# Kernel optimization log

Hardware: AMD Instinct MI355X
Metric: run time of the kernel (lower is better)

## Reference

```python
import jax, jax.numpy as jnp
import numpy as np

EMB = 256
HEADS = 2
IMG = 224
P1, P2 = 16, 8
LN_EPS = 1e-5


def _layer_norm(t, g, b):
    m = jnp.mean(t, axis=-1, keepdims=True)
    v = jnp.mean((t - m) ** 2, axis=-1, keepdims=True)
    return (t - m) * jax.lax.rsqrt(v + LN_EPS) * g + b


def _patch_embed(x, W, b, cls_tok, p):
    B, C, H, Wd = x.shape
    h, w = H // p, Wd // p
    # b c (h p1)(w p2) -> b (h w) (p1 p2 c)
    t = x.reshape(B, C, h, p, w, p).transpose(0, 2, 4, 3, 5, 1).reshape(B, h * w, p * p * C)
    t = t @ W + b
    cls = jnp.broadcast_to(cls_tok, (B, 1, cls_tok.shape[-1]))
    return jnp.concatenate([cls, t], axis=1)


def setup_inputs() -> dict:
    key = jax.random.key(0)
    ks = jax.random.split(key, 16)
    s = 0.02
    d = {
        "x": jax.random.normal(ks[0], (128, 3, IMG, IMG), dtype=jnp.float32),
        "W1": jax.random.normal(ks[1], (P1 * P1 * 3, EMB), dtype=jnp.float32) * s,
        "b1": jnp.zeros((EMB,), jnp.float32),
        "cls1": jax.random.normal(ks[2], (1, 1, EMB), dtype=jnp.float32),
        "W2": jax.random.normal(ks[3], (P2 * P2 * 3, EMB), dtype=jnp.float32) * s,
        "b2": jnp.zeros((EMB,), jnp.float32),
        "cls2": jax.random.normal(ks[4], (1, 1, EMB), dtype=jnp.float32),
        "ln1_g": jnp.ones((EMB,), jnp.float32),
        "ln1_b": jnp.zeros((EMB,), jnp.float32),
        "Wq": jax.random.normal(ks[5], (EMB, EMB), dtype=jnp.float32) * s,
        "bq": jnp.zeros((EMB,), jnp.float32),
        "Wk": jax.random.normal(ks[6], (EMB, EMB), dtype=jnp.float32) * s,
        "bk": jnp.zeros((EMB,), jnp.float32),
        "Wv": jax.random.normal(ks[7], (EMB, EMB), dtype=jnp.float32) * s,
        "bv": jnp.zeros((EMB,), jnp.float32),
        "Wp": jax.random.normal(ks[8], (EMB, EMB), dtype=jnp.float32) * s,
        "bp": jnp.zeros((EMB,), jnp.float32),
        "ln2_g": jnp.ones((EMB,), jnp.float32),
        "ln2_b": jnp.zeros((EMB,), jnp.float32),
        "lnc_g": jnp.ones((EMB,), jnp.float32),
        "lnc_b": jnp.zeros((EMB,), jnp.float32),
        "Wc": jax.random.normal(ks[9], (EMB, 2), dtype=jnp.float32) * s,
        "bc": jnp.zeros((2,), jnp.float32),
    }
    return d


def reference(x, W1, b1, cls1, W2, b2, cls2, ln1_g, ln1_b, Wq, bq, Wk, bk, Wv, bv,
              Wp, bp, ln2_g, ln2_b, lnc_g, lnc_b, Wc, bc):
    B = x.shape[0]
    p1 = _patch_embed(x, W1, b1, cls1, P1)   # [B, 197, 256]
    p2 = _patch_embed(x, W2, b2, cls2, P2)   # [B, 785, 256]
    n = p1.shape[1]
    idx = jnp.linspace(0.0, p2.shape[1] - 1, n).astype(jnp.int32)  # truncation like .long()
    p2r = p2[:, idx, :]
    z = jnp.concatenate([p2r, p1], axis=1)   # [B, 394, 256]
    N = z.shape[1]

    h = _layer_norm(z, ln1_g, ln1_b)
    dh = EMB // HEADS
    q = (h @ Wq + bq).reshape(B, N, HEADS, dh).transpose(0, 2, 1, 3)
    k = (h @ Wk + bk).reshape(B, N, HEADS, dh).transpose(0, 2, 1, 3)
    v = (h @ Wv + bv).reshape(B, N, HEADS, dh).transpose(0, 2, 1, 3)
    attn = jnp.einsum('bhqd,bhkd->bhqk', q, k)
    # NOTE: faithful to source — softmax of UNscaled logits, then divide by sqrt(emb)
    attn = jax.nn.softmax(attn, axis=-1) / (EMB ** 0.5)
    o = jnp.einsum('bhqk,bhkd->bhqd', attn, v).transpose(0, 2, 1, 3).reshape(B, N, EMB)
    o = o @ Wp + bp
    o = _layer_norm(o, ln2_g, ln2_b)
    z = z + o

    pooled = jnp.mean(z, axis=1)
    logits = _layer_norm(pooled, lnc_g, lnc_b) @ Wc + bc
    return jax.nn.log_softmax(logits, axis=1)
```

## Files before the change

### kernel.cpp

```cpp
#include <hip/hip_runtime.h>

typedef short short8 __attribute__((ext_vector_type(8)));
typedef float f32x4 __attribute__((ext_vector_type(4)));
typedef unsigned short us4 __attribute__((ext_vector_type(4)));
typedef unsigned short u16;

#define MFMA(a,b,c) __builtin_amdgcn_mfma_f32_16x16x32_bf16((a),(b),(c),0,0,0)

__device__ __forceinline__ u16 f2b(float f) {
    union { float f; unsigned int i; } v; v.f = f;
    unsigned int x = v.i;
    return (u16)((x + 0x7fffu + ((x >> 16) & 1u)) >> 16);
}

__device__ __forceinline__ unsigned int pk2(float lo, float hi) {
    return (unsigned int)f2b(lo) | ((unsigned int)f2b(hi) << 16);
}

__global__ __launch_bounds__(256) void k_wtrans(const float* __restrict__ W1,
        const float* __restrict__ W2, const float* __restrict__ Wq, const float* __restrict__ Wk,
        const float* __restrict__ Wv, const float* __restrict__ Wp,
        u16* __restrict__ w1t, u16* __restrict__ w2t, u16* __restrict__ wqt,
        u16* __restrict__ wkt, u16* __restrict__ wvt, u16* __restrict__ wpt) {
    int bx = blockIdx.x, n = threadIdx.x;
    if (bx < 768) {
        int k = bx, c = k % 3, t = k / 3, pj = t & 15, pi = t >> 4;
        int kp2 = c*256 + pi*16 + pj;
        w1t[(size_t)(kp2 >> 5)*8192 + n*32 + (kp2 & 31)] = f2b(W1[(size_t)k*256 + n]);
    } else if (bx < 960) {
        int k = bx - 768, c = k % 3, t = k / 3, pj = t & 7, pi = t >> 3;
        int kp2 = c*64 + pi*8 + pj;
        w2t[(size_t)(kp2 >> 5)*8192 + n*32 + (kp2 & 31)] = f2b(W2[(size_t)k*256 + n]);
    } else if (bx < 1216) { int k = bx - 960;  wqt[(size_t)(k>>5)*8192 + n*32 + (k&31)] = f2b(Wq[(size_t)k*256 + n]); }
    else if (bx < 1472)   { int k = bx - 1216; wkt[(size_t)(k>>5)*8192 + n*32 + (k&31)] = f2b(Wk[(size_t)k*256 + n]); }
    else if (bx < 1728)   { int k = bx - 1472; wvt[(size_t)(k>>5)*8192 + n*32 + (k&31)] = f2b(Wv[(size_t)k*256 + n]); }
    else                  { int k = bx - 1728; wpt[(size_t)(k>>5)*8192 + n*32 + (k&31)] = f2b(Wp[(size_t)k*256 + n]); }
}

__global__ __launch_bounds__(256) void k_cls(const float* __restrict__ cls1,
        const float* __restrict__ cls2, const float* __restrict__ g1, const float* __restrict__ be1,
        float* __restrict__ z, u16* __restrict__ h) {
    __shared__ float red[16];
    int b = blockIdx.x, e = threadIdx.x, lane = e & 63, w = e >> 6;
    float v0 = cls2[e], v1 = cls1[e];
    z[((size_t)b*394 + 0)*256 + e]   = v0;
    z[((size_t)b*394 + 197)*256 + e] = v1;
    float s0 = v0, q0 = v0*v0, s1 = v1, q1 = v1*v1;
    #pragma unroll
    for (int m = 1; m < 64; m <<= 1) {
        s0 += __shfl_xor(s0, m); q0 += __shfl_xor(q0, m);
        s1 += __shfl_xor(s1, m); q1 += __shfl_xor(q1, m);
    }
    if (lane == 0) { red[w] = s0; red[4+w] = q0; red[8+w] = s1; red[12+w] = q1; }
    __syncthreads();
    float S0 = red[0]+red[1]+red[2]+red[3],   Q0 = red[4]+red[5]+red[6]+red[7];
    float S1 = red[8]+red[9]+red[10]+red[11], Q1 = red[12]+red[13]+red[14]+red[15];
    float m0 = S0*(1.f/256.f), r0 = rsqrtf(Q0*(1.f/256.f) - m0*m0 + 1e-5f);
    float m1 = S1*(1.f/256.f), r1 = rsqrtf(Q1*(1.f/256.f) - m1*m1 + 1e-5f);
    h[((size_t)b*394 + 0)*256 + e]   = f2b((v0-m0)*r0*g1[e] + be1[e]);
    h[((size_t)b*394 + 197)*256 + e] = f2b((v1-m1)*r1*g1[e] + be1[e]);
}

__global__ __launch_bounds__(256) void k_im2col1(const float* __restrict__ x,
        u16* __restrict__ A1) {
    int b = blockIdx.y, g = blockIdx.x, tid = threadIdx.x;
    int p = tid >> 4, pi = tid & 15;
    int j = g*16 + p;
    u16* dst = A1 + ((size_t)b*208 + j)*768;
    if (j < 196) {
        int hi = j / 14, wi = j - hi*14;
        #pragma unroll
        for (int c = 0; c < 3; ++c) {
            const float* src = x + (((size_t)b*3 + c)*224 + hi*16 + pi)*224 + wi*16;
            f32x4 r0 = *(const f32x4*)(src);
            f32x4 r1 = *(const f32x4*)(src + 4);
            f32x4 r2 = *(const f32x4*)(src + 8);
            f32x4 r3 = *(const f32x4*)(src + 12);
            union { u16 u[16]; uint4 q[2]; } t;
            #pragma unroll
            for (int s = 0; s < 4; ++s) {
                t.u[s] = f2b(r0[s]); t.u[4+s] = f2b(r1[s]);
                t.u[8+s] = f2b(r2[s]); t.u[12+s] = f2b(r3[s]);
            }
            *(uint4*)&dst[c*256 + pi*16] = t.q[0];
            *(uint4*)&dst[c*256 + pi*16 + 8] = t.q[1];
        }
    } else {
        uint4 zer = {0,0,0,0};
        #pragma unroll
        for (int c = 0; c < 3; ++c) {
            *(uint4*)&dst[c*256 + pi*16] = zer;
            *(uint4*)&dst[c*256 + pi*16 + 8] = zer;
        }
    }
}

__global__ __launch_bounds__(256) void k_embed1(const u16* __restrict__ A1,
        const u16* __restrict__ w1t, const float* __restrict__ b1,
        const float* __restrict__ g1, const float* __restrict__ be1,
        float* __restrict__ z, u16* __restrict__ h, int nrows) {
    __shared__ __align__(16) u16 Ab[2][64*40];
    __shared__ __align__(16) u16 Bb[2][256*40];
    __shared__ float red[64][8];
    int tid = threadIdx.x;
    int r0 = blockIdx.x * 64;
    int w = tid >> 6, lane = tid & 63, quad = lane >> 4, tf = lane & 15;
    int arow = tid >> 2, aoff = (tid & 3) * 8;
    const u16* ap = A1 + (size_t)(r0 + arow)*768 + aoff;
    uint4 ra  = *(const uint4*)(ap);
    uint4 rb0 = *(const uint4*)&w1t[tid*8];
    uint4 rb1 = *(const uint4*)&w1t[2048 + tid*8];
    uint4 rb2 = *(const uint4*)&w1t[4096 + tid*8];
    uint4 rb3 = *(const uint4*)&w1t[6144 + tid*8];
    f32x4 zero = {0.f,0.f,0.f,0.f};
    f32x4 acc[4][4];
    #pragma unroll
    for (int m = 0; m < 4; ++m)
        #pragma unroll
        for (int nf = 0; nf < 4; ++nf) acc[m][nf] = zero;
    #pragma unroll
    for (int kc = 0; kc < 24; ++kc) {
        int buf = kc & 1;
        *(uint4*)&Ab[buf][arow*40 + aoff] = ra;
        *(uint4*)&Bb[buf][(arow      )*40 + aoff] = rb0;
        *(uint4*)&Bb[buf][(arow +  64)*40 + aoff] = rb1;
        *(uint4*)&Bb[buf][(arow + 128)*40 + aoff] = rb2;
        *(uint4*)&Bb[buf][(arow + 192)*40 + aoff] = rb3;
        int nc = kc < 23 ? kc + 1 : 23;
        ra = *(const uint4*)(ap + nc*32);
        const u16* src = w1t + (size_t)nc*8192;
        rb0 = *(const uint4*)&src[tid*8];
        rb1 = *(const uint4*)&src[2048 + tid*8];
        rb2 = *(const uint4*)&src[4096 + tid*8];
        rb3 = *(const uint4*)&src[6144 + tid*8];
        __syncthreads();
        short8 a0 = *(const short8*)&Ab[buf][(     tf)*40 + quad*8];
        short8 a1 = *(const short8*)&Ab[buf][(16 + tf)*40 + quad*8];
        short8 a2 = *(const short8*)&Ab[buf][(32 + tf)*40 + quad*8];
        short8 a3 = *(const short8*)&Ab[buf][(48 + tf)*40 + quad*8];
        #pragma unroll
        for (int nf = 0; nf < 4; ++nf) {
            short8 bb = *(const short8*)&Bb[buf][(w*64 + nf*16 + tf)*40 + quad*8];
            acc[0][nf] = MFMA(a0, bb, acc[0][nf]);
            acc[1][nf] = MFMA(a1, bb, acc[1][nf]);
            acc[2][nf] = MFMA(a2, bb, acc[2][nf]);
            acc[3][nf] = MFMA(a3, bb, acc[3][nf]);
        }
    }
    float bias[4], gv[4], bev[4];
    #pragma unroll
    for (int nf = 0; nf < 4; ++nf) {
        int n = w*64 + nf*16 + tf;
        bias[nf] = b1[n]; gv[nf] = g1[n]; bev[nf] = be1[n];
    }
    #pragma unroll
    for (int m = 0; m < 4; ++m)
        #pragma unroll
        for (int nf = 0; nf < 4; ++nf)
            #pragma unroll
            for (int i = 0; i < 4; ++i) acc[m][nf][i] += bias[nf];
    #pragma unroll
    for (int m = 0; m < 4; ++m)
        #pragma unroll
        for (int i = 0; i < 4; ++i) {
            float s = acc[m][0][i] + acc[m][1][i] + acc[m][2][i] + acc[m][3][i];
            float qv = acc[m][0][i]*acc[m][0][i] + acc[m][1][i]*acc[m][1][i]
                     + acc[m][2][i]*acc[m][2][i] + acc[m][3][i]*acc[m][3][i];
            #pragma unroll
            for (int d = 1; d < 16; d <<= 1) { s += __shfl_xor(s, d); qv += __shfl_xor(qv, d); }
            if (tf == 0) {
                red[m*16 + quad*4 + i][w] = s;
                red[m*16 + quad*4 + i][4 + w] = qv;
            }
        }
    __syncthreads();
    #pragma unroll
    for (int m = 0; m < 4; ++m)
        #pragma unroll
        for (int i = 0; i < 4; ++i) {
            int rl = m*16 + quad*4 + i;
            float S = red[rl][0]+red[rl][1]+red[rl][2]+red[rl][3];
            float Q = red[rl][4]+red[rl][5]+red[rl][6]+red[rl][7];
            float mean = S*(1.f/256.f);
            float rs = rsqrtf(Q*(1.f/256.f) - mean*mean + 1e-5f);
            int row = r0 + rl;
            if (row < nrows) {
                int img = row / 208;
                int j = row - img*208;
                if (j < 196) {
                    size_t base = ((size_t)img*394 + 198 + j)*256;
                    #pragma unroll
                    for (int nf = 0; nf < 4; ++nf) {
                        int n = w*64 + nf*16 + tf;
                        float v = acc[m][nf][i];
                        z[base + n] = v;
                        h[base + n] = f2b((v - mean)*rs*gv[nf] + bev[nf]);
                    }
                }
            }
        }
}

__global__ __launch_bounds__(256) void k_embed2(const float* __restrict__ x,
        const u16* __restrict__ w2t, const float* __restrict__ b2,
        const float* __restrict__ g1, const float* __restrict__ be1,
        float* __restrict__ z, u16* __restrict__ h) {
    __shared__ __align__(16) u16 A[16*200];
    __shared__ __align__(16) u16 Wst[8192];
    __shared__ __align__(16) float S[16*260];
    int b = blockIdx.y, g = blockIdx.x, tid = threadIdx.x;
    int p = tid >> 4, s16 = tid & 15;
    int pi = s16 >> 1, ph = s16 & 1;
    int it = g*16 + p + 1;
    uint4 wr0 = *(const uint4*)&w2t[tid*8];
    uint4 wr1 = *(const uint4*)&w2t[2048 + tid*8];
    uint4 wr2 = *(const uint4*)&w2t[4096 + tid*8];
    uint4 wr3 = *(const uint4*)&w2t[6144 + tid*8];
    auto stage = [&](const u16* base, int chunk) {
        __syncthreads();
        *(uint4*)&Wst[tid*8] = wr0;
        *(uint4*)&Wst[2048 + tid*8] = wr1;
        *(uint4*)&Wst[4096 + tid*8] = wr2;
        *(uint4*)&Wst[6144 + tid*8] = wr3;
        __syncthreads();
        if (base) {
            const u16* src = base + (size_t)chunk*8192;
            wr0 = *(const uint4*)&src[tid*8];
            wr1 = *(const uint4*)&src[2048 + tid*8];
            wr2 = *(const uint4*)&src[4096 + tid*8];
            wr3 = *(const uint4*)&src[6144 + tid*8];
        }
    };
    if (it <= 196) {
        int patch = 4*it - 1;
        int hi = patch / 28, wi = patch - hi*28;
        #pragma unroll
        for (int c = 0; c < 3; ++c) {
            const float* src = x + (((size_t)b*3 + c)*224 + hi*8 + pi)*224 + wi*8 + ph*4;
            f32x4 r = *(const f32x4*)src;
            us4 o; o[0] = f2b(r[0]); o[1] = f2b(r[1]); o[2] = f2b(r[2]); o[3] = f2b(r[3]);
            *(us4*)&A[p*200 + c*64 + pi*8 + ph*4] = o;
        }
    } else {
        us4 zer = {0,0,0,0};
        #pragma unroll
        for (int c = 0; c < 3; ++c)
            *(us4*)&A[p*200 + c*64 + pi*8 + ph*4] = zer;
    }
    int w = tid >> 6, lane = tid & 63, quad = lane >> 4, tf = lane & 15;
    f32x4 zero = {0.f,0.f,0.f,0.f};
    f32x4 acc[4] = {zero,zero,zero,zero};
    #pragma unroll
    for (int ks = 0; ks < 6; ++ks) {
        stage(ks < 5 ? w2t : nullptr, ks + 1);
        short8 a = *(const short8*)&A[tf*200 + ks*32 + quad*8];
        #pragma unroll
        for (int nf = 0; nf < 4; ++nf) {
            short8 bb = *(const short8*)&Wst[(w*64 + nf*16 + tf)*32 + quad*8];
            acc[nf] = MFMA(a, bb, acc[nf]);
        }
    }
    #pragma unroll
    for (int nf = 0; nf < 4; ++nf) {
        int n = w*64 + nf*16 + tf;
        float bias = b2[n];
        #pragma unroll
        for (int i = 0; i < 4; ++i)
            S[(quad*4 + i)*260 + n] = acc[nf][i] + bias;
    }
    __syncthreads();
    #pragma unroll
    for (int rr = 0; rr < 4; ++rr) {
        int row = w*4 + rr;
        int it2 = g*16 + row + 1;
        f32x4 v = *(const f32x4*)&S[row*260 + lane*4];
        float s = v[0]+v[1]+v[2]+v[3];
        float sq = v[0]*v[0]+v[1]*v[1]+v[2]*v[2]+v[3]*v[3];
        #pragma unroll
        for (int m = 1; m < 64; m <<= 1) { s += __shfl_xor(s, m); sq += __shfl_xor(sq, m); }
        float mean = s*(1.f/256.f);
        float rs = rsqrtf(sq*(1.f/256.f) - mean*mean + 1e-5f);
        if (it2 <= 196) {
            size_t base = ((size_t)b*394 + it2)*256 + lane*4;
            *(f32x4*)&z[base] = v;
            us4 ho;
            #pragma unroll
            for (int c = 0; c < 4; ++c) {
                int e = lane*4 + c;
                ho[c] = f2b((v[c]-mean)*rs*g1[e] + be1[e]);
            }
            *(us4*)&h[base] = ho;
        }
    }
}

__device__ __forceinline__ void store_qk(f32x4 acc[4][4], const float* __restrict__ bs,
        u16* __restrict__ dst, u16* Sst, int b, int mt, int w, int quad, int tf, int tid) {
    #pragma unroll
    for (int m = 0; m < 4; ++m) {
        __syncthreads();
        #pragma unroll
        for (int nf = 0; nf < 4; ++nf) {
            int e = w*64 + nf*16 + tf;
            float bias = bs[e];
            #pragma unroll
            for (int i = 0; i < 4; ++i) {
                int n = mt*64 + m*16 + quad*4 + i;
                Sst[(quad*4 + i)*264 + e] = (n < 394) ? f2b(acc[m][nf][i] + bias) : (u16)0;
            }
        }
        __syncthreads();
        int row = tid >> 4, c16 = tid & 15;
        int n = mt*64 + m*16 + row;
        if (n < 416) {
            int e0 = c16*16, hh = e0 >> 7, d0 = e0 & 127;
            uint4 v0 = *(const uint4*)&Sst[row*264 + e0];
            uint4 v1 = *(const uint4*)&Sst[row*264 + e0 + 8];
            u16* p = dst + ((size_t)(b*2 + hh)*416 + n)*128 + d0;
            *(uint4*)p = v0;
            *(uint4*)(p + 8) = v1;
        }
    }
}

__device__ __forceinline__ void store_v(f32x4 acc[4][4], const float* __restrict__ bs,
        u16* __restrict__ vt, u16* Sst, int b, int mt, int w, int quad, int tf, int tid) {
    #pragma unroll
    for (int nf = 0; nf < 4; ++nf) {
        __syncthreads();
        #pragma unroll
        for (int i = 0; i < 4; ++i) {
            int e = w*64 + nf*16 + quad*4 + i;
            float bias = bs[e];
            #pragma unroll
            for (int m = 0; m < 4; ++m) {
                int n = mt*64 + m*16 + tf;
                Sst[(w*16 + quad*4 + i)*72 + m*16 + tf] = (n < 394) ? f2b(acc[m][nf][i] + bias) : (u16)0;
            }
        }
        __syncthreads();
        #pragma unroll
        for (int k = 0; k < 2; ++k) {
            int ch = tid + k*256;
            int row = ch >> 3, c8 = ch & 7;
            int n0 = mt*64 + c8*8;
            if (n0 < 416) {
                int e = (row >> 4)*64 + nf*16 + (row & 15);
                int d = e & 127, hh = e >> 7;
                uint4 v = *(const uint4*)&Sst[row*72 + c8*8];
                *(uint4*)&vt[((size_t)(b*2 + hh)*128 + d)*416 + n0] = v;
            }
        }
    }
}

__global__ __launch_bounds__(256) void k_qkv(const u16* __restrict__ h,
        const u16* __restrict__ wqt, const u16* __restrict__ wkt, const u16* __restrict__ wvt,
        const float* __restrict__ bq, const float* __restrict__ bk, const float* __restrict__ bv,
        u16* __restrict__ q, u16* __restrict__ kb, u16* __restrict__ vt) {
    __shared__ __align__(16) u16 A[64*264];
    __shared__ __align__(16) u16 Wst[2][8192];
    __shared__ __align__(16) u16 Sst[4608];
    int mt = blockIdx.x, b = blockIdx.y, tid = threadIdx.x;
    uint4 wr0 = *(const uint4*)&wqt[tid*8];
    uint4 wr1 = *(const uint4*)&wqt[2048 + tid*8];
    uint4 wr2 = *(const uint4*)&wqt[4096 + tid*8];
    uint4 wr3 = *(const uint4*)&wqt[6144 + tid*8];
    auto wwrite = [&](int buf) {
        *(uint4*)&Wst[buf][tid*8] = wr0;
        *(uint4*)&Wst[buf][2048 + tid*8] = wr1;
        *(uint4*)&Wst[buf][4096 + tid*8] = wr2;
        *(uint4*)&Wst[buf][6144 + tid*8] = wr3;
    };
    auto wload = [&](const u16* src) {
        wr0 = *(const uint4*)&src[tid*8];
        wr1 = *(const uint4*)&src[2048 + tid*8];
        wr2 = *(const uint4*)&src[4096 + tid*8];
        wr3 = *(const uint4*)&src[6144 + tid*8];
    };
    #pragma unroll
    for (int it = 0; it < 8; ++it) {
        int idx = tid + it*256;
        int row = idx >> 5, seg = idx & 31;
        int n = mt*64 + row;
        uint4 val = {0,0,0,0};
        if (n < 394) val = *(const uint4*)&h[((size_t)b*394 + n)*256 + seg*8];
        *(uint4*)&A[row*264 + seg*8] = val;
    }
    int w = tid >> 6, lane = tid & 63, quad = lane >> 4, tf = lane & 15;
    f32x4 zero = {0.f,0.f,0.f,0.f};

    {
        f32x4 acc[4][4];
        #pragma unroll
        for (int m = 0; m < 4; ++m)
            #pragma unroll
            for (int nf = 0; nf < 4; ++nf) acc[m][nf] = zero;
        #pragma unroll
        for (int ks = 0; ks < 8; ++ks) {
            int buf = ks & 1;
            wwrite(buf);
            wload(ks < 7 ? wqt + (size_t)(ks+1)*8192 : wkt);
            __syncthreads();
            short8 a0 = *(const short8*)&A[tf*264 + ks*32 + quad*8];
            short8 a1 = *(const short8*)&A[(16+tf)*264 + ks*32 + quad*8];
            short8 a2 = *(const short8*)&A[(32+tf)*264 + ks*32 + quad*8];
            short8 a3 = *(const short8*)&A[(48+tf)*264 + ks*32 + quad*8];
            #pragma unroll
            for (int nf = 0; nf < 4; ++nf) {
                short8 bb = *(const short8*)&Wst[buf][(w*64 + nf*16 + tf)*32 + quad*8];
                acc[0][nf] = MFMA(a0, bb, acc[0][nf]);
                acc[1][nf] = MFMA(a1, bb, acc[1][nf]);
                acc[2][nf] = MFMA(a2, bb, acc[2][nf]);
                acc[3][nf] = MFMA(a3, bb, acc[3][nf]);
            }
        }
        store_qk(acc, bq, q, Sst, b, mt, w, quad, tf, tid);
    }
    {
        f32x4 acc[4][4];
        #pragma unroll
        for (int m = 0; m < 4; ++m)
            #pragma unroll
            for (int nf = 0; nf < 4; ++nf) acc[m][nf] = zero;
        #pragma unroll
        for (int ks = 0; ks < 8; ++ks) {
            int buf = ks & 1;
            wwrite(buf);
            wload(ks < 7 ? wkt + (size_t)(ks+1)*8192 : wvt);
            __syncthreads();
            short8 a0 = *(const short8*)&A[tf*264 + ks*32 + quad*8];
            short8 a1 = *(const short8*)&A[(16+tf)*264 + ks*32 + quad*8];
            short8 a2 = *(const short8*)&A[(32+tf)*264 + ks*32 + quad*8];
            short8 a3 = *(const short8*)&A[(48+tf)*264 + ks*32 + quad*8];
            #pragma unroll
            for (int nf = 0; nf < 4; ++nf) {
                short8 bb = *(const short8*)&Wst[buf][(w*64 + nf*16 + tf)*32 + quad*8];
                acc[0][nf] = MFMA(a0, bb, acc[0][nf]);
                acc[1][nf] = MFMA(a1, bb, acc[1][nf]);
                acc[2][nf] = MFMA(a2, bb, acc[2][nf]);
                acc[3][nf] = MFMA(a3, bb, acc[3][nf]);
            }
        }
        store_qk(acc, bk, kb, Sst, b, mt, w, quad, tf, tid);
    }
    {
        f32x4 acc[4][4];
        #pragma unroll
        for (int m = 0; m < 4; ++m)
            #pragma unroll
            for (int nf = 0; nf < 4; ++nf) acc[m][nf] = zero;
        #pragma unroll
        for (int ks = 0; ks < 8; ++ks) {
            int buf = ks & 1;
            wwrite(buf);
            if (ks < 7) wload(wvt + (size_t)(ks+1)*8192);
            __syncthreads();
            short8 a0 = *(const short8*)&A[tf*264 + ks*32 + quad*8];
            short8 a1 = *(const short8*)&A[(16+tf)*264 + ks*32 + quad*8];
            short8 a2 = *(const short8*)&A[(32+tf)*264 + ks*32 + quad*8];
            short8 a3 = *(const short8*)&A[(48+tf)*264 + ks*32 + quad*8];
            #pragma unroll
            for (int nf = 0; nf < 4; ++nf) {
                short8 bb = *(const short8*)&Wst[buf][(w*64 + nf*16 + tf)*32 + quad*8];
                acc[0][nf] = MFMA(bb, a0, acc[0][nf]);
                acc[1][nf] = MFMA(bb, a1, acc[1][nf]);
                acc[2][nf] = MFMA(bb, a2, acc[2][nf]);
                acc[3][nf] = MFMA(bb, a3, acc[3][nf]);
            }
        }
        store_v(acc, bv, vt, Sst, b, mt, w, quad, tf, tid);
    }
}

__global__ __launch_bounds__(256) void k_att(const u16* __restrict__ q,
        const u16* __restrict__ kbuf, const u16* __restrict__ vt, u16* __restrict__ o) {
    __shared__ __align__(16) u16 pool[18944];
    int nwg = gridDim.x * gridDim.y;
    int orig = blockIdx.y * gridDim.x + blockIdx.x;
    int q8 = nwg >> 3, r8 = nwg & 7;
    int xcd = orig & 7, idx = orig >> 3;
    int nid = (xcd < r8 ? xcd*(q8+1) : r8*(q8+1) + (xcd-r8)*q8) + idx;
    int bx = nid % 7, bh = nid / 7;
    int tid = threadIdx.x;
    int w = tid >> 6, lane = tid & 63, quad = lane >> 4, tf = lane & 15;
    int mt_raw = bx*4 + w;
    int mt = mt_raw < 26 ? mt_raw : 25;
    const u16* qp = q    + (size_t)bh*53248;
    const u16* kp = kbuf + (size_t)bh*53248;
    const u16* vp = vt   + (size_t)bh*53248;
    short8 afr[4];
    #pragma unroll
    for (int ks = 0; ks < 4; ++ks)
        afr[ks] = *(const short8*)&qp[(size_t)(mt*16 + tf)*128 + ks*32 + quad*8];
    f32x4 zero = {0.f,0.f,0.f,0.f};
    f32x4 acc[25];
    #pragma unroll
    for (int nt = 0; nt < 25; ++nt) acc[nt] = zero;
    int sr0 = tid >> 4, sseg = tid & 15;
    uint4 kreg0 = *(const uint4*)&kp[(size_t)sr0*128 + sseg*8];
    uint4 kreg1 = *(const uint4*)&kp[(size_t)(sr0+16)*128 + sseg*8];
    for (int kc = 0; kc < 13; ++kc) {
        u16* K = pool + (kc & 1)*4352;
        *(uint4*)&K[sr0*136 + sseg*8] = kreg0;
        *(uint4*)&K[(sr0+16)*136 + sseg*8] = kreg1;
        if (kc < 12) {
            kreg0 = *(const uint4*)&kp[(size_t)((kc+1)*32 + sr0)*128 + sseg*8];
            kreg1 = *(const uint4*)&kp[(size_t)((kc+1)*32 + sr0 + 16)*128 + sseg*8];
        }
        __syncthreads();
        #pragma unroll
        for (int ncl = 0; ncl < 2; ++ncl) {
            int nt = kc*2 + ncl;
            if (nt < 25) {
                #pragma unroll
                for (int ks = 0; ks < 4; ++ks) {
                    short8 kk = *(const short8*)&K[(ncl*16 + tf)*136 + ks*32 + quad*8];
                    acc[nt] = MFMA(kk, afr[ks], acc[nt]);
                }
            }
        }
    }
    int vd0 = tid >> 2, vseg = tid & 3;
    uint4 vreg0 = *(const uint4*)&vp[(size_t)vd0*416 + vseg*8];
    uint4 vreg1 = *(const uint4*)&vp[(size_t)(vd0+64)*416 + vseg*8];
    float mx = -3e38f;
    #pragma unroll
    for (int nt = 0; nt < 24; ++nt)
        #pragma unroll
        for (int i = 0; i < 4; ++i) mx = fmaxf(mx, acc[nt][i]);
    #pragma unroll
    for (int i = 0; i < 4; ++i)
        if (quad*4 + i < 10) mx = fmaxf(mx, acc[24][i]);
    mx = fmaxf(mx, __shfl_xor(mx, 16));
    mx = fmaxf(mx, __shfl_xor(mx, 32));
    float s = 0.f;
    #pragma unroll
    for (int nt = 0; nt < 24; ++nt)
        #pragma unroll
        for (int i = 0; i < 4; ++i) {
            float e = __expf(acc[nt][i] - mx);
            acc[nt][i] = e; s += e;
        }
    #pragma unroll
    for (int i = 0; i < 4; ++i) {
        if (quad*4 + i < 10) { float e = __expf(acc[24][i] - mx); acc[24][i] = e; s += e; }
        else acc[24][i] = 0.f;
    }
    s += __shfl_xor(s, 16);
    s += __shfl_xor(s, 32);
    float inv = 1.f / (16.f * s);
    #pragma unroll
    for (int nt = 0; nt < 25; ++nt)
        #pragma unroll
        for (int i = 0; i < 4; ++i) acc[nt][i] *= inv;
    f32x4 acc2[8];
    #pragma unroll
    for (int nf = 0; nf < 8; ++nf) acc2[nf] = zero;
    int qb0 = quad & 1;
    int g = (qb0 << 1) | (quad >> 1);
    for (int kc = 0; kc < 13; ++kc) {
        u16* V = pool + 8704 + (kc & 1)*5120;
        *(uint4*)&V[vd0*40 + vseg*8] = vreg0;
        *(uint4*)&V[(vd0+64)*40 + vseg*8] = vreg1;
        if (kc < 12) {
            vreg0 = *(const uint4*)&vp[(size_t)vd0*416 + (kc+1)*32 + vseg*8];
            vreg1 = *(const uint4*)&vp[(size_t)(vd0+64)*416 + (kc+1)*32 + vseg*8];
        }
        __syncthreads();
        f32x4 v0 = acc[2*kc];
        f32x4 v1 = (kc < 12) ? acc[2*kc + 1] : zero;
        unsigned int r0 = pk2(v0[0], v0[1]);
        unsigned int r1 = pk2(v0[2], v0[3]);
        unsigned int r2 = pk2(v1[0], v1[1]);
        unsigned int r3 = pk2(v1[2], v1[3]);
        unsigned int sa = qb0 ? r0 : r2, sb = qb0 ? r1 : r3;
        unsigned int ra = (unsigned int)__shfl_xor((int)sa, 16);
        unsigned int rb = (unsigned int)__shfl_xor((int)sb, 16);
        unsigned int ka = qb0 ? r2 : r0, kb2 = qb0 ? r3 : r1;
        union { unsigned int u[4]; short8 s8; } au;
        au.u[0] = qb0 ? ra : ka;
        au.u[1] = qb0 ? rb : kb2;
        au.u[2] = qb0 ? ka : ra;
        au.u[3] = qb0 ? kb2 : rb;
        short8 a = au.s8;
        #pragma unroll
        for (int nf = 0; nf < 8; ++nf) {
            short8 bb = *(const short8*)&V[(nf*16 + tf)*40 + g*8];
            acc2[nf] = MFMA(a, bb, acc2[nf]);
        }
    }
    int b = bh >> 1, hh = bh & 1;
    __syncthreads();
    #pragma unroll
    for (int nf = 0; nf < 8; ++nf)
        #pragma unroll
        for (int i = 0; i < 4; ++i)
            pool[w*2176 + (quad*4 + i)*136 + nf*16 + tf] = f2b(acc2[nf][i]);
    __syncthreads();
    if (mt_raw < 26) {
        #pragma unroll
        for (int r4 = 0; r4 < 4; ++r4) {
            int rr = r4*4 + (lane >> 4);
            int n = mt_raw*16 + rr;
            if (n < 394) {
                int c16 = lane & 15;
                uint4 v = *(const uint4*)&pool[w*2176 + rr*136 + c16*8];
                *(uint4*)&o[((size_t)b*394 + n)*256 + hh*128 + c16*8] = v;
            }
        }
    }
}

__global__ __launch_bounds__(256) void k_proj(const u16* __restrict__ o,
        const u16* __restrict__ wpt, const float* __restrict__ bp,
        const float* __restrict__ g2, const float* __restrict__ bb2,
        float* __restrict__ z) {
    __shared__ __align__(16) u16 A[32*264];
    __shared__ __align__(16) u16 Wst[8192];
    __shared__ __align__(16) float S[32*260];
    int mt = blockIdx.x, b = blockIdx.y, tid = threadIdx.x;
    int w = tid >> 6, lane = tid & 63, quad = lane >> 4, tf = lane & 15;
    uint4 wr0 = *(const uint4*)&wpt[tid*8];
    uint4 wr1 = *(const uint4*)&wpt[2048 + tid*8];
    uint4 wr2 = *(const uint4*)&wpt[4096 + tid*8];
    uint4 wr3 = *(const uint4*)&wpt[6144 + tid*8];
    auto stage = [&](const u16* base, int chunk) {
        __syncthreads();
        *(uint4*)&Wst[tid*8] = wr0;
        *(uint4*)&Wst[2048 + tid*8] = wr1;
        *(uint4*)&Wst[4096 + tid*8] = wr2;
        *(uint4*)&Wst[6144 + tid*8] = wr3;
        __syncthreads();
        if (base) {
            const u16* src = base + (size_t)chunk*8192;
            wr0 = *(const uint4*)&src[tid*8];
            wr1 = *(const uint4*)&src[2048 + tid*8];
            wr2 = *(const uint4*)&src[4096 + tid*8];
            wr3 = *(const uint4*)&src[6144 + tid*8];
        }
    };
    for (int idx = tid; idx < 2048; idx += 256) {
        int row = idx >> 6, col4 = (idx & 63) * 4;
        int n = mt*32 + row;
        us4 val = {0,0,0,0};
        if (n < 394) val = *(const us4*)&o[((size_t)b*394 + n)*256 + col4];
        *(us4*)&A[row*264 + col4] = val;
    }
    f32x4 zero = {0.f,0.f,0.f,0.f};
    f32x4 acc[2][4];
    #pragma unroll
    for (int m = 0; m < 2; ++m)
        #pragma unroll
        for (int nf = 0; nf < 4; ++nf) acc[m][nf] = zero;
    #pragma unroll
    for (int ks = 0; ks < 8; ++ks) {
        stage(ks < 7 ? wpt : nullptr, ks + 1);
        short8 a0 = *(const short8*)&A[tf*264 + ks*32 + quad*8];
        short8 a1 = *(const short8*)&A[(16+tf)*264 + ks*32 + quad*8];
        #pragma unroll
        for (int nf = 0; nf < 4; ++nf) {
            short8 bb = *(const short8*)&Wst[(w*64 + nf*16 + tf)*32 + quad*8];
            acc[0][nf] = MFMA(a0, bb, acc[0][nf]);
            acc[1][nf] = MFMA(a1, bb, acc[1][nf]);
        }
    }
    #pragma unroll
    for (int nf = 0; nf < 4; ++nf) {
        int e = w*64 + nf*16 + tf;
        float bsv = bp[e];
        #pragma unroll
        for (int m = 0; m < 2; ++m)
            #pragma unroll
            for (int i = 0; i < 4; ++i)
                S[(m*16 + quad*4 + i)*260 + e] = acc[m][nf][i] + bsv;
    }
    __syncthreads();
    #pragma unroll
    for (int rr = 0; rr < 8; ++rr) {
        int row = w*8 + rr;
        f32x4 v = *(const f32x4*)&S[row*260 + lane*4];
        float s = v[0]+v[1]+v[2]+v[3];
        float sq = v[0]*v[0]+v[1]*v[1]+v[2]*v[2]+v[3]*v[3];
        #pragma unroll
        for (int m = 1; m < 64; m <<= 1) { s += __shfl_xor(s, m); sq += __shfl_xor(sq, m); }
        float mean = s*(1.f/256.f);
        float rs = rsqrtf(sq*(1.f/256.f) - mean*mean + 1e-5f);
        int n = mt*32 + row;
        if (n < 394) {
            float* zr = z + ((size_t)b*394 + n)*256 + lane*4;
            f32x4 zv = *(f32x4*)zr;
            #pragma unroll
            for (int c = 0; c < 4; ++c) {
                int e = lane*4 + c;
                zv[c] += (v[c]-mean)*rs*g2[e] + bb2[e];
            }
            *(f32x4*)zr = zv;
        }
    }
}

__global__ __launch_bounds__(256) void k_poolsum(const float* __restrict__ z,
        float* __restrict__ partial) {
    int g = blockIdx.x, b = blockIdx.y, e = threadIdx.x;
    int nb = gridDim.y;
    int n0 = g*99, n1 = 394 < n0+99 ? 394 : n0+99;
    const float* zp = z + (size_t)b*394*256 + e;
    float p0 = 0.f, p1 = 0.f, p2 = 0.f, p3 = 0.f;
    int n = n0;
    for (; n + 3 < n1; n += 4) {
        p0 += zp[(size_t)n*256];       p1 += zp[(size_t)(n+1)*256];
        p2 += zp[(size_t)(n+2)*256];   p3 += zp[(size_t)(n+3)*256];
    }
    for (; n < n1; ++n) p0 += zp[(size_t)n*256];
    partial[((size_t)g*nb + b)*256 + e] = (p0+p1)+(p2+p3);
}

__global__ __launch_bounds__(256) void k_pool2(const float* __restrict__ partial,
        const float* __restrict__ lg, const float* __restrict__ lb,
        const float* __restrict__ wc, const float* __restrict__ bc,
        float* __restrict__ out, int nb) {
    __shared__ float red[8];
    int b = blockIdx.x, e = threadIdx.x;
    int wave = e >> 6, lane = e & 63;
    float pooled = (partial[((size_t)0*nb + b)*256 + e] + partial[((size_t)1*nb + b)*256 + e]
                  + partial[((size_t)2*nb + b)*256 + e] + partial[((size_t)3*nb + b)*256 + e])
                 * (1.f/394.f);
    float a = pooled, sq = pooled*pooled;
    #pragma unroll
    for (int m = 1; m < 64; m <<= 1) { a += __shfl_xor(a, m); sq += __shfl_xor(sq, m); }
    if (lane == 0) { red[wave] = a; red[4+wave] = sq; }
    __syncthreads();
    float tot = red[0]+red[1]+red[2]+red[3];
    float totq = red[4]+red[5]+red[6]+red[7];
    float mean = tot*(1.f/256.f);
    float rs = rsqrtf(totq*(1.f/256.f) - mean*mean + 1e-5f);
    float ln = (pooled-mean)*rs*lg[e] + lb[e];
    float t0 = ln * wc[e*2], t1 = ln * wc[e*2+1];
    #pragma unroll
    for (int m = 1; m < 64; m <<= 1) { t0 += __shfl_xor(t0, m); t1 += __shfl_xor(t1, m); }
    __syncthreads();
    if (lane == 0) { red[wave] = t0; red[4+wave] = t1; }
    __syncthreads();
    if (e < 2) {
        float l0 = red[0]+red[1]+red[2]+red[3] + bc[0];
        float l1 = red[4]+red[5]+red[6]+red[7] + bc[1];
        float mx = fmaxf(l0, l1);
        float lse = mx + logf(__expf(l0-mx) + __expf(l1-mx));
        out[b*2 + e] = (e == 0 ? l0 : l1) - lse;
    }
}

extern "C" void kernel_launch(void* const* d_in, const int* in_sizes, int n_in,
                              void* d_out, int out_size, void* d_ws, size_t ws_size,
                              hipStream_t stream) {
    const float* x    = (const float*)d_in[0];
    const float* W1   = (const float*)d_in[1];
    const float* b1   = (const float*)d_in[2];
    const float* cls1 = (const float*)d_in[3];
    const float* W2   = (const float*)d_in[4];
    const float* b2   = (const float*)d_in[5];
    const float* cls2 = (const float*)d_in[6];
    const float* ln1g = (const float*)d_in[7];
    const float* ln1b = (const float*)d_in[8];
    const float* Wq   = (const float*)d_in[9];
    const float* bq   = (const float*)d_in[10];
    const float* Wk   = (const float*)d_in[11];
    const float* bk   = (const float*)d_in[12];
    const float* Wv   = (const float*)d_in[13];
    const float* bv   = (const float*)d_in[14];
    const float* Wp   = (const float*)d_in[15];
    const float* bp   = (const float*)d_in[16];
    const float* ln2g = (const float*)d_in[17];
    const float* ln2b = (const float*)d_in[18];
    const float* lncg = (const float*)d_in[19];
    const float* lncb = (const float*)d_in[20];
    const float* Wc   = (const float*)d_in[21];
    const float* bcp  = (const float*)d_in[22];

    int Bn = in_sizes[0] / (3*224*224);

    const size_t WBYTES = 1015808;
    const size_t PER_IMG = 403456 + 201728 + 212992*3 + 4096;
    size_t avail = (ws_size > WBYTES) ? ws_size - WBYTES : 0;
    int Bc = (int)(avail / PER_IMG);
    if (Bc < 1) Bc = 1;
    if (Bc > Bn) Bc = Bn;

    u16* w1t = (u16*)d_ws;
    u16* w2t = w1t + 196608;
    u16* wqt = w2t + 49152;
    u16* wkt = wqt + 65536;
    u16* wvt = wkt + 65536;
    u16* wpt = wvt + 65536;
    float* z = (float*)(wpt + 65536);
    u16* h   = (u16*)(z + (size_t)Bc*100864);
    u16* o   = h;
    u16* q   = h + (size_t)Bc*100864;
    u16* kb  = q + (size_t)Bc*106496;
    u16* vt  = kb + (size_t)Bc*106496;
    float* partial = (float*)(vt + (size_t)Bc*106496);

    k_wtrans<<<1984, 256, 0, stream>>>(W1, W2, Wq, Wk, Wv, Wp, w1t, w2t, wqt, wkt, wvt, wpt);

    for (int b0 = 0; b0 < Bn; b0 += Bc) {
        int bc = (Bn - b0 < Bc) ? (Bn - b0) : Bc;
        const float* xb = x + (size_t)b0 * 3*224*224;
        float* outb = (float*)d_out + (size_t)b0 * 2;
        int nrows = bc * 208;
        int gm = (nrows + 63) / 64;

        k_cls<<<bc, 256, 0, stream>>>(cls1, cls2, ln1g, ln1b, z, h);
        k_im2col1<<<dim3(13, bc), 256, 0, stream>>>(xb, q );
        k_embed1<<<gm, 256, 0, stream>>>(q , w1t, b1, ln1g, ln1b, z, h, nrows);
        k_embed2<<<dim3(13, bc), 256, 0, stream>>>(xb, w2t, b2, ln1g, ln1b, z, h);
        k_qkv<<<dim3(7, bc), 256, 0, stream>>>(h, wqt, wkt, wvt, bq, bk, bv, q, kb, vt);
        k_att<<<dim3(7, bc*2), 256, 0, stream>>>(q, kb, vt, o);
        k_proj<<<dim3(13, bc), 256, 0, stream>>>(o, wpt, bp, ln2g, ln2b, z);
        k_poolsum<<<dim3(4, bc), 256, 0, stream>>>(z, partial);
        k_pool2<<<bc, 256, 0, stream>>>(partial, lncg, lncb, Wc, bcp, outb, bc);
    }
}
```

Before: 379.9 us.

## Deepen register prefetch to two stages in embed, QKV and attention loops

Global-to-register prefetch in the embed1 GEMM, the QKV projection and the attention K/V streaming loops now runs two chunks ahead instead of one, using two register sets. This gives global loads a full extra iteration to land before they are written to LDS, which helps hide memory latency. The attention loops are also fully unrolled. The cost is extra VGPRs (another set of uint4 registers on top of large accumulator arrays, especially the 25-tile attention accumulator), which may reduce occupancy or cause spills.

```diff
diff --git a/kernel.cpp b/kernel.cpp
--- a/kernel.cpp
+++ b/kernel.cpp
@@ -107,11 +107,18 @@
     int w = tid >> 6, lane = tid & 63, quad = lane >> 4, tf = lane & 15;
     int arow = tid >> 2, aoff = (tid & 3) * 8;
     const u16* ap = A1 + (size_t)(r0 + arow)*768 + aoff;
-    uint4 ra  = *(const uint4*)(ap);
-    uint4 rb0 = *(const uint4*)&w1t[tid*8];
-    uint4 rb1 = *(const uint4*)&w1t[2048 + tid*8];
-    uint4 rb2 = *(const uint4*)&w1t[4096 + tid*8];
-    uint4 rb3 = *(const uint4*)&w1t[6144 + tid*8];
+    uint4 ra[2];
+    uint4 rb[2][4];
+    auto pload = [&](int set, int c) {
+        ra[set] = *(const uint4*)(ap + c*32);
+        const u16* src = w1t + (size_t)c*8192;
+        rb[set][0] = *(const uint4*)&src[tid*8];
+        rb[set][1] = *(const uint4*)&src[2048 + tid*8];
+        rb[set][2] = *(const uint4*)&src[4096 + tid*8];
+        rb[set][3] = *(const uint4*)&src[6144 + tid*8];
+    };
+    pload(0, 0);
+    pload(1, 1);
     f32x4 zero = {0.f,0.f,0.f,0.f};
     f32x4 acc[4][4];
     #pragma unroll
@@ -121,18 +128,12 @@
     #pragma unroll
     for (int kc = 0; kc < 24; ++kc) {
         int buf = kc & 1;
-        *(uint4*)&Ab[buf][arow*40 + aoff] = ra;
-        *(uint4*)&Bb[buf][(arow      )*40 + aoff] = rb0;
-        *(uint4*)&Bb[buf][(arow +  64)*40 + aoff] = rb1;
-        *(uint4*)&Bb[buf][(arow + 128)*40 + aoff] = rb2;
-        *(uint4*)&Bb[buf][(arow + 192)*40 + aoff] = rb3;
-        int nc = kc < 23 ? kc + 1 : 23;
-        ra = *(const uint4*)(ap + nc*32);
-        const u16* src = w1t + (size_t)nc*8192;
-        rb0 = *(const uint4*)&src[tid*8];
-        rb1 = *(const uint4*)&src[2048 + tid*8];
-        rb2 = *(const uint4*)&src[4096 + tid*8];
-        rb3 = *(const uint4*)&src[6144 + tid*8];
+        *(uint4*)&Ab[buf][arow*40 + aoff] = ra[buf];
+        *(uint4*)&Bb[buf][(arow      )*40 + aoff] = rb[buf][0];
+        *(uint4*)&Bb[buf][(arow +  64)*40 + aoff] = rb[buf][1];
+        *(uint4*)&Bb[buf][(arow + 128)*40 + aoff] = rb[buf][2];
+        *(uint4*)&Bb[buf][(arow + 192)*40 + aoff] = rb[buf][3];
+        if (kc + 2 < 24) pload(buf, kc + 2);
         __syncthreads();
         short8 a0 = *(const short8*)&Ab[buf][(     tf)*40 + quad*8];
         short8 a1 = *(const short8*)&Ab[buf][(16 + tf)*40 + quad*8];
@@ -362,22 +363,23 @@
     __shared__ __align__(16) u16 Wst[2][8192];
     __shared__ __align__(16) u16 Sst[4608];
     int mt = blockIdx.x, b = blockIdx.y, tid = threadIdx.x;
-    uint4 wr0 = *(const uint4*)&wqt[tid*8];
-    uint4 wr1 = *(const uint4*)&wqt[2048 + tid*8];
-    uint4 wr2 = *(const uint4*)&wqt[4096 + tid*8];
-    uint4 wr3 = *(const uint4*)&wqt[6144 + tid*8];
-    auto wwrite = [&](int buf) {
-        *(uint4*)&Wst[buf][tid*8] = wr0;
-        *(uint4*)&Wst[buf][2048 + tid*8] = wr1;
-        *(uint4*)&Wst[buf][4096 + tid*8] = wr2;
-        *(uint4*)&Wst[buf][6144 + tid*8] = wr3;
+    const u16* srcs[3] = {wqt, wkt, wvt};
+    uint4 wreg[2][4];
+    auto wload = [&](int set, int i) {
+        const u16* src = srcs[i >> 3] + (size_t)(i & 7)*8192;
+        wreg[set][0] = *(const uint4*)&src[tid*8];
+        wreg[set][1] = *(const uint4*)&src[2048 + tid*8];
+        wreg[set][2] = *(const uint4*)&src[4096 + tid*8];
+        wreg[set][3] = *(const uint4*)&src[6144 + tid*8];
     };
-    auto wload = [&](const u16* src) {
-        wr0 = *(const uint4*)&src[tid*8];
-        wr1 = *(const uint4*)&src[2048 + tid*8];
-        wr2 = *(const uint4*)&src[4096 + tid*8];
-        wr3 = *(const uint4*)&src[6144 + tid*8];
+    auto wwrite = [&](int buf, int set) {
+        *(uint4*)&Wst[buf][tid*8] = wreg[set][0];
+        *(uint4*)&Wst[buf][2048 + tid*8] = wreg[set][1];
+        *(uint4*)&Wst[buf][4096 + tid*8] = wreg[set][2];
+        *(uint4*)&Wst[buf][6144 + tid*8] = wreg[set][3];
     };
+    wload(0, 0);
+    wload(1, 1);
     #pragma unroll
     for (int it = 0; it < 8; ++it) {
         int idx = tid + it*256;
@@ -398,9 +400,9 @@
             for (int nf = 0; nf < 4; ++nf) acc[m][nf] = zero;
         #pragma unroll
         for (int ks = 0; ks < 8; ++ks) {
-            int buf = ks & 1;
-            wwrite(buf);
-            wload(ks < 7 ? wqt + (size_t)(ks+1)*8192 : wkt);
+            int i = ks, buf = i & 1;
+            wwrite(buf, buf);
+            if (i + 2 < 24) wload(buf, i + 2);
             __syncthreads();
             short8 a0 = *(const short8*)&A[tf*264 + ks*32 + quad*8];
             short8 a1 = *(const short8*)&A[(16+tf)*264 + ks*32 + quad*8];
@@ -425,9 +427,9 @@
             for (int nf = 0; nf < 4; ++nf) acc[m][nf] = zero;
         #pragma unroll
         for (int ks = 0; ks < 8; ++ks) {
-            int buf = ks & 1;
-            wwrite(buf);
-            wload(ks < 7 ? wkt + (size_t)(ks+1)*8192 : wvt);
+            int i = 8 + ks, buf = i & 1;
+            wwrite(buf, buf);
+            if (i + 2 < 24) wload(buf, i + 2);
             __syncthreads();
             short8 a0 = *(const short8*)&A[tf*264 + ks*32 + quad*8];
             short8 a1 = *(const short8*)&A[(16+tf)*264 + ks*32 + quad*8];
@@ -452,9 +454,9 @@
             for (int nf = 0; nf < 4; ++nf) acc[m][nf] = zero;
         #pragma unroll
         for (int ks = 0; ks < 8; ++ks) {
-            int buf = ks & 1;
-            wwrite(buf);
-            if (ks < 7) wload(wvt + (size_t)(ks+1)*8192);
+            int i = 16 + ks, buf = i & 1;
+            wwrite(buf, buf);
+            if (i + 2 < 24) wload(buf, i + 2);
             __syncthreads();
             short8 a0 = *(const short8*)&A[tf*264 + ks*32 + quad*8];
             short8 a1 = *(const short8*)&A[(16+tf)*264 + ks*32 + quad*8];
@@ -498,16 +500,20 @@
     #pragma unroll
     for (int nt = 0; nt < 25; ++nt) acc[nt] = zero;
     int sr0 = tid >> 4, sseg = tid & 15;
-    uint4 kreg0 = *(const uint4*)&kp[(size_t)sr0*128 + sseg*8];
-    uint4 kreg1 = *(const uint4*)&kp[(size_t)(sr0+16)*128 + sseg*8];
+    uint4 kreg[2][2];
+    auto kload = [&](int set, int kc) {
+        kreg[set][0] = *(const uint4*)&kp[(size_t)(kc*32 + sr0)*128 + sseg*8];
+        kreg[set][1] = *(const uint4*)&kp[(size_t)(kc*32 + sr0 + 16)*128 + sseg*8];
+    };
+    kload(0, 0);
+    kload(1, 1);
+    #pragma unroll
     for (int kc = 0; kc < 13; ++kc) {
-        u16* K = pool + (kc & 1)*4352;
-        *(uint4*)&K[sr0*136 + sseg*8] = kreg0;
-        *(uint4*)&K[(sr0+16)*136 + sseg*8] = kreg1;
-        if (kc < 12) {
-            kreg0 = *(const uint4*)&kp[(size_t)((kc+1)*32 + sr0)*128 + sseg*8];
-            kreg1 = *(const uint4*)&kp[(size_t)((kc+1)*32 + sr0 + 16)*128 + sseg*8];
-        }
+        int buf = kc & 1;
+        u16* K = pool + buf*4352;
+        *(uint4*)&K[sr0*136 + sseg*8] = kreg[buf][0];
+        *(uint4*)&K[(sr0+16)*136 + sseg*8] = kreg[buf][1];
+        if (kc + 2 < 13) kload(buf, kc + 2);
         __syncthreads();
         #pragma unroll
         for (int ncl = 0; ncl < 2; ++ncl) {
@@ -522,8 +528,13 @@
         }
     }
     int vd0 = tid >> 2, vseg = tid & 3;
-    uint4 vreg0 = *(const uint4*)&vp[(size_t)vd0*416 + vseg*8];
-    uint4 vreg1 = *(const uint4*)&vp[(size_t)(vd0+64)*416 + vseg*8];
+    uint4 vreg[2][2];
+    auto vload = [&](int set, int kc) {
+        vreg[set][0] = *(const uint4*)&vp[(size_t)vd0*416 + kc*32 + vseg*8];
+        vreg[set][1] = *(const uint4*)&vp[(size_t)(vd0+64)*416 + kc*32 + vseg*8];
+    };
+    vload(0, 0);
+    vload(1, 1);
     float mx = -3e38f;
     #pragma unroll
     for (int nt = 0; nt < 24; ++nt)
@@ -559,14 +570,13 @@
     for (int nf = 0; nf < 8; ++nf) acc2[nf] = zero;
     int qb0 = quad & 1;
     int g = (qb0 << 1) | (quad >> 1);
+    #pragma unroll
     for (int kc = 0; kc < 13; ++kc) {
-        u16* V = pool + 8704 + (kc & 1)*5120;
-        *(uint4*)&V[vd0*40 + vseg*8] = vreg0;
-        *(uint4*)&V[(vd0+64)*40 + vseg*8] = vreg1;
-        if (kc < 12) {
-            vreg0 = *(const uint4*)&vp[(size_t)vd0*416 + (kc+1)*32 + vseg*8];
-            vreg1 = *(const uint4*)&vp[(size_t)(vd0+64)*416 + (kc+1)*32 + vseg*8];
-        }
+        int buf = kc & 1;
+        u16* V = pool + 8704 + buf*5120;
+        *(uint4*)&V[vd0*40 + vseg*8] = vreg[buf][0];
+        *(uint4*)&V[(vd0+64)*40 + vseg*8] = vreg[buf][1];
+        if (kc + 2 < 13) vload(buf, kc + 2);
         __syncthreads();
         f32x4 v0 = acc[2*kc];
         f32x4 v1 = (kc < 12) ? acc[2*kc + 1] : zero;
```

After: 560.6 us. 1.48x slower.
